# Kernel tuning notes

Measured on AMD Instinct MI355X. Metric: run time of the kernel, lower is better.

Reference implementation:

```python
import jax, jax.numpy as jnp
import numpy as np

N_QUBITS = 12
BATCH = 4096


def _rx(t):
    c = jnp.cos(t / 2).astype(jnp.complex64)
    s = jnp.sin(t / 2).astype(jnp.complex64)
    return jnp.stack([jnp.stack([c, -1j * s], -1), jnp.stack([-1j * s, c], -1)], -2)


def _ry(t):
    c = jnp.cos(t / 2).astype(jnp.complex64)
    s = jnp.sin(t / 2).astype(jnp.complex64)
    return jnp.stack([jnp.stack([c, -s], -1), jnp.stack([s, c], -1)], -2)


def _rz(t):
    e0 = jnp.exp(-0.5j * t.astype(jnp.complex64))
    e1 = jnp.exp(0.5j * t.astype(jnp.complex64))
    z = jnp.zeros_like(e0)
    return jnp.stack([jnp.stack([e0, z], -1), jnp.stack([z, e1], -1)], -2)


ISWAP = jnp.array([[1, 0, 0, 0], [0, 0, 1j, 0], [0, 1j, 0, 0], [0, 0, 0, 1]], dtype=jnp.complex64)


def apply_1q(state, mat, wire):
    # state: [B] + [2]*n, mat: [2,2] or [B,2,2]
    state = jnp.moveaxis(state, wire + 1, 1)
    if mat.ndim == 3:
        state = jnp.einsum('bij,bj...->bi...', mat, state)
    else:
        state = jnp.einsum('ij,bj...->bi...', mat, state)
    return jnp.moveaxis(state, 1, wire + 1)


def apply_2q(state, mat4, w0, w1):
    state = jnp.moveaxis(state, (w0 + 1, w1 + 1), (1, 2))
    shp = state.shape
    state = state.reshape(shp[0], 4, -1)
    state = jnp.einsum('ij,bjr->bir', mat4, state)
    return jnp.moveaxis(state.reshape(shp), (1, 2), (w0 + 1, w1 + 1))


def setup_inputs() -> dict:
    key = jax.random.key(0)
    k1, k2, k3 = jax.random.split(key, 3)
    x = jax.random.normal(k1, (BATCH, 1, 14, 14), dtype=jnp.float32)
    conv_w = jax.random.uniform(k2, (1, 1, 4, 4), jnp.float32, 0.0, 0.1)
    conv_b = jax.random.uniform(k3, (1,), jnp.float32, 0.01, 1.0)
    theta = jnp.full((3,), np.pi / 2, dtype=jnp.float32)  # trainable RX/RY/RZ angles
    return {"x": x, "conv_w": conv_w, "conv_b": conv_b, "theta": theta}


def _circuit(f, theta):
    # f: [B, 36] encoding angles
    B = f.shape[0]
    state = jnp.zeros((B,) + (2,) * N_QUBITS, jnp.complex64)
    state = state.at[(slice(None),) + (0,) * N_QUBITS].set(1.0)
    # encoder1: gates [rx, ry, rx] per qubit, angle = f[:, q*3+i]
    gates1 = (_rx, _ry, _rx)
    for q in range(N_QUBITS):
        for i in range(3):
            state = apply_1q(state, gates1[i](f[:, q * 3 + i]), q)
    # iswap ascending: wires [11,10], [10,9], ..., [1,0]
    for i in range(N_QUBITS - 1):
        state = apply_2q(state, ISWAP, N_QUBITS - i - 1, N_QUBITS - i - 2)
    # encoder2: gates [ry, rx, ry]
    gates2 = (_ry, _rx, _ry)
    for q in range(N_QUBITS):
        for i in range(3):
            state = apply_1q(state, gates2[i](f[:, q * 3 + i]), q)
    # iswap descending: wires [1,0], [2,1], ..., [11,10]
    for i in range(N_QUBITS - 1):
        state = apply_2q(state, ISWAP, i + 1, i)
    # trainable rotations on wires 0 then 1 (shared params)
    for w in (0, 1):
        state = apply_1q(state, _rx(theta[0]), w)
        state = apply_1q(state, _ry(theta[1]), w)
        state = apply_1q(state, _rz(theta[2]), w)
    probs = state.real ** 2 + state.imag ** 2  # [B] + [2]*12
    outs = []
    for w in (0, 1):  # <Z> on wires 0, 1
        p = jnp.moveaxis(probs, w + 1, 1).reshape(B, 2, -1).sum(-1)
        outs.append(p[:, 0] - p[:, 1])
    return jnp.stack(outs, -1)  # [B, 2]


def reference(x, conv_w, conv_b, theta):
    feats = jax.lax.conv_general_dilated(
        x, conv_w, window_strides=(2, 2), padding='VALID',
        dimension_numbers=('NCHW', 'OIHW', 'NCHW')) + conv_b[None, :, None, None]
    f = feats.reshape(x.shape[0], -1)  # [B, 36]
    return _circuit(f, theta)
```

## Files before the change

kernel.cpp:

```cpp
#include <hip/hip_runtime.h>

#define THREADS 64
#define EPB 16

__device__ __forceinline__ float2 cmul(float2 a, float2 b) {
    return make_float2(a.x * b.x - a.y * b.y, a.x * b.y + a.y * b.x);
}
__device__ __forceinline__ float2 cadd(float2 a, float2 b) { return make_float2(a.x + b.x, a.y + b.y); }
__device__ __forceinline__ float2 csub(float2 a, float2 b) { return make_float2(a.x - b.x, a.y - b.y); }
__device__ __forceinline__ float2 conjc(float2 a) { return make_float2(a.x, -a.y); }
__device__ __forceinline__ float2 cmuli(float2 a) { return make_float2(-a.y, a.x); }
__device__ __forceinline__ float2 cdot(float2 a, float2 b) {
    return make_float2(a.x * b.x + a.y * b.y, a.x * b.y - a.y * b.x);
}
__device__ __forceinline__ float2 cscale(float s, float2 a) { return make_float2(s * a.x, s * a.y); }

__device__ __forceinline__ void mat_rx(float c, float s, float2 m[4]) {
    m[0] = make_float2(c, 0.f);  m[1] = make_float2(0.f, -s);
    m[2] = make_float2(0.f, -s); m[3] = make_float2(c, 0.f);
}
__device__ __forceinline__ void mat_ry(float c, float s, float2 m[4]) {
    m[0] = make_float2(c, 0.f);  m[1] = make_float2(-s, 0.f);
    m[2] = make_float2(s, 0.f);  m[3] = make_float2(c, 0.f);
}
__device__ __forceinline__ void mmul(const float2 A[4], const float2 B[4], float2 C[4]) {
    C[0] = cadd(cmul(A[0], B[0]), cmul(A[1], B[2]));
    C[1] = cadd(cmul(A[0], B[1]), cmul(A[1], B[3]));
    C[2] = cadd(cmul(A[2], B[0]), cmul(A[3], B[2]));
    C[3] = cadd(cmul(A[2], B[1]), cmul(A[3], B[3]));
}

__device__ __forceinline__ float2 shfl2(float2 a, int src) {
    return make_float2(__shfl(a.x, src), __shfl(a.y, src));
}
__device__ __forceinline__ float2 shflx2(float2 a, int mask) {
    return make_float2(__shfl_xor(a.x, mask), __shfl_xor(a.y, mask));
}

__global__ __launch_bounds__(THREADS) void qcnn_closed4(
    const float* __restrict__ x,
    const float* __restrict__ cw,
    const float* __restrict__ cb,
    const float* __restrict__ th,
    float* __restrict__ out,
    int B)
{
    __shared__ float xs[EPB][197];

    const int tid = threadIdx.x;
    const int sub = tid & 3;
    const int grp = tid >> 2;
    const int b   = blockIdx.x * EPB + grp;

    const float th0 = th[0], th1 = th[1];

    {
        const float4* xv = (const float4*)(x + (size_t)blockIdx.x * EPB * 196);
        float4 v[12];
#pragma unroll
        for (int k = 0; k < 12; ++k) v[k] = xv[tid + k * THREADS];
        float4 vt;
        if (tid < 16) vt = xv[768 + tid];
#pragma unroll
        for (int k = 0; k < 12; ++k) {
            int i4 = tid + k * THREADS;
            int r  = i4 / 49;
            int c  = (i4 - r * 49) * 4;
            xs[r][c + 0] = v[k].x;
            xs[r][c + 1] = v[k].y;
            xs[r][c + 2] = v[k].z;
            xs[r][c + 3] = v[k].w;
        }
        if (tid < 16) {
            int i4 = 768 + tid;
            int r  = i4 / 49;
            int c  = (i4 - r * 49) * 4;
            xs[r][c + 0] = vt.x;
            xs[r][c + 1] = vt.y;
            xs[r][c + 2] = vt.z;
            xs[r][c + 3] = vt.w;
        }
    }

    float o00; float2 o01;
    {
        float ct0 = __cosf(0.5f * th0), st0v = __sinf(0.5f * th0);
        float ct1 = __cosf(0.5f * th1), st1v = __sinf(0.5f * th1);
        float2 Rx[4], Ry[4], M[4];
        mat_rx(ct0, st0v, Rx); mat_ry(ct1, st1v, Ry); mmul(Ry, Rx, M);
        o00 = (M[0].x * M[0].x + M[0].y * M[0].y)
            - (M[2].x * M[2].x + M[2].y * M[2].y);
        o01 = csub(cmul(conjc(M[0]), M[1]), cmul(conjc(M[2]), M[3]));
    }

    float wgt[16];
#pragma unroll
    for (int k = 0; k < 16; ++k) wgt[k] = cw[k];
    const float bias = cb[0];

    __syncthreads();
    const float* row = xs[grp];

    float ang[9];
#pragma unroll
    for (int m = 0; m < 9; ++m) {
        int o  = sub * 9 + m;
        int oy = o / 6, ox = o % 6;
        float acc = bias;
#pragma unroll
        for (int ky = 0; ky < 4; ++ky)
#pragma unroll
            for (int kx = 0; kx < 4; ++kx)
                acc += row[(2 * oy + ky) * 14 + (2 * ox + kx)] * wgt[ky * 4 + kx];
        ang[m] = acc;
    }

    float2 u[3][2];
    float2 V[3][4];
#pragma unroll
    for (int j = 0; j < 3; ++j) {
        float c0 = __cosf(0.5f * ang[3 * j + 0]), s0 = __sinf(0.5f * ang[3 * j + 0]);
        float c1 = __cosf(0.5f * ang[3 * j + 1]), s1 = __sinf(0.5f * ang[3 * j + 1]);
        float c2 = __cosf(0.5f * ang[3 * j + 2]), s2 = __sinf(0.5f * ang[3 * j + 2]);
        {
            float2 b0c = make_float2(c0, 0.f);
            float2 b1c = make_float2(0.f, -s0);
            float2 t0 = csub(cscale(c1, b0c), cscale(s1, b1c));
            float2 t1 = cadd(cscale(s1, b0c), cscale(c1, b1c));
            u[j][0] = cadd(cscale(c2, t0), cmul(make_float2(0.f, -s2), t1));
            u[j][1] = cadd(cmul(make_float2(0.f, -s2), t0), cscale(c2, t1));
        }
        {
            float2 A[4], Bm[4], Cm[4], T[4];
            mat_ry(c0, s0, A); mat_rx(c1, s1, Bm); mat_ry(c2, s2, Cm);
            mmul(Bm, A, T); mmul(Cm, T, V[j]);
        }
    }

    const int srcPrev = tid - (sub ? 1 : 0);
    float2 up0 = shfl2(u[2][0], srcPrev);
    float2 up1 = shfl2(u[2][1], srcPrev);

    float2 P0p[2][2], P1p[2][2];
#pragma unroll
    for (int v = 0; v < 2; ++v)
#pragma unroll
        for (int vp = 0; vp < 2; ++vp) {
            P0p[v][vp] = make_float2(1.f, 0.f);
            P1p[v][vp] = make_float2(1.f, 0.f);
        }
    float2 V0[4], h9[2][2], h10[2][2];

#pragma unroll
    for (int j = 0; j < 3; ++j) {
        float2 pv0 = (j == 0) ? up0 : u[j - 1][0];
        float2 pv1 = (j == 0) ? up1 : u[j - 1][1];
        float2 hc[2][2];
#pragma unroll
        for (int v = 0; v < 2; ++v) {
            float2 g0 = (v == 0) ? pv0 : cmuli(pv0);
            float2 g1 = (v == 1) ? pv1 : cmuli(pv1);
            hc[v][0] = cadd(cmul(V[j][0], g0), cmul(V[j][1], g1));
            hc[v][1] = cadd(cmul(V[j][2], g0), cmul(V[j][3], g1));
        }
        float2 S[2][2];
#pragma unroll
        for (int v = 0; v < 2; ++v)
#pragma unroll
            for (int vp = 0; vp < 2; ++vp)
                S[v][vp] = cadd(cdot(hc[v][0], hc[vp][0]),
                                cdot(hc[v][1], hc[vp][1]));

        if (sub == 0) {
            if (j == 0) {
#pragma unroll
                for (int k = 0; k < 4; ++k) V0[k] = V[0][k];
            } else if (j == 1) {
#pragma unroll
                for (int v = 0; v < 2; ++v) {
                    h10[v][0] = hc[v][0]; h10[v][1] = hc[v][1];
#pragma unroll
                    for (int vp = 0; vp < 2; ++vp)
                        P1p[v][vp] = cmul(P1p[v][vp], S[v][vp]);
                }
            } else {
#pragma unroll
                for (int v = 0; v < 2; ++v) {
                    h9[v][0] = hc[v][0]; h9[v][1] = hc[v][1];
#pragma unroll
                    for (int vp = 0; vp < 2; ++vp)
                        P0p[v][vp] = cmul(P0p[v][vp], S[v][vp]);
                }
            }
        } else {
#pragma unroll
            for (int v = 0; v < 2; ++v)
#pragma unroll
                for (int vp = 0; vp < 2; ++vp) {
                    P0p[v][vp] = cmul(P0p[v][vp], S[v][vp]);
                    P1p[v][vp] = cmul(P1p[v][vp], S[v][vp]);
                }
        }
    }

#pragma unroll
    for (int d = 1; d <= 2; d <<= 1) {
#pragma unroll
        for (int v = 0; v < 2; ++v)
#pragma unroll
            for (int vp = 0; vp < 2; ++vp) {
                P0p[v][vp] = cmul(P0p[v][vp], shflx2(P0p[v][vp], d));
                P1p[v][vp] = cmul(P1p[v][vp], shflx2(P1p[v][vp], d));
            }
    }

    const int srcLast = tid | 3;
    float2 u11_0 = shfl2(u[2][0], srcLast);
    float2 u11_1 = shfl2(u[2][1], srcLast);

    if (sub == 0) {
        float2 h11[2][2];
        h11[0][0] = cmul(u11_0, V0[0]); h11[0][1] = cmul(u11_0, V0[2]);
        h11[1][0] = cmul(u11_1, V0[1]); h11[1][1] = cmul(u11_1, V0[3]);

        float2 E0 = make_float2(0.f, 0.f), E1 = make_float2(0.f, 0.f);
#pragma unroll
        for (int w = 0; w < 2; ++w) {
            float2 Ow01 = (w == 0) ? cmuli(o01) : make_float2(o01.y, -o01.x);
            float2 Ow10 = conjc(Ow01);
#pragma unroll
            for (int v = 0; v < 2; ++v) {
#pragma unroll
                for (int vp = 0; vp < 2; ++vp) {
                    float2 A = cdot(h11[v][w], h11[vp][w]);
                    float2 T0 = cadd(cadd(
                        cscale(o00, csub(cdot(h10[v][0], h10[vp][0]),
                                         cdot(h10[v][1], h10[vp][1]))),
                        cmul(Ow01, cdot(h10[v][0], h10[vp][1]))),
                        cmul(Ow10, cdot(h10[v][1], h10[vp][0])));
                    float2 T1 = cadd(cadd(
                        cscale(o00, csub(cdot(h9[v][0], h9[vp][0]),
                                         cdot(h9[v][1], h9[vp][1]))),
                        cmul(Ow01, cdot(h9[v][0], h9[vp][1]))),
                        cmul(Ow10, cdot(h9[v][1], h9[vp][0])));
                    E0 = cadd(E0, cmul(cmul(A, T0), P0p[v][vp]));
                    E1 = cadd(E1, cmul(cmul(A, T1), P1p[v][vp]));
                }
            }
        }
        if (b < B)
            ((float2*)out)[b] = make_float2(E0.x, E1.x);
    }
}

extern "C" void kernel_launch(void* const* d_in, const int* in_sizes, int n_in,
                              void* d_out, int out_size, void* d_ws, size_t ws_size,
                              hipStream_t stream) {
    const float* x  = (const float*)d_in[0];
    const float* cw = (const float*)d_in[1];
    const float* cb = (const float*)d_in[2];
    const float* th = (const float*)d_in[3];
    float* out = (float*)d_out;
    int B = in_sizes[0] / 196;
    qcnn_closed4<<<B / EPB, THREADS, 0, stream>>>(x, cw, cb, th, out, B);
}
```

Measured before the change: 11.01 us.

## Load image rows directly into registers instead of staging through shared memory

Each thread now loads the 6 image rows (84 floats) it needs straight from global memory into registers, then computes 12 conv outputs and picks 9 based on sub parity. This removes the shared-memory tile and the __syncthreads barrier. In exchange every row is loaded by several threads, each thread does 12 instead of 9 convolutions, and register pressure rises sharply (84 floats) with uncoalesced per-thread float4 loads.

```diff
diff --git a/kernel.cpp b/kernel.cpp
--- a/kernel.cpp
+++ b/kernel.cpp
@@ -45,43 +45,27 @@
     float* __restrict__ out,
     int B)
 {
-    __shared__ float xs[EPB][197];
-
     const int tid = threadIdx.x;
     const int sub = tid & 3;
     const int grp = tid >> 2;
     const int b   = blockIdx.x * EPB + grp;
 
+    const int r0 = (sub * 3) & ~1;
+    const float* src = x + (size_t)b * 196 + r0 * 14;
+    float arr[84];
+    {
+        const float4* sv = (const float4*)src;
+#pragma unroll
+        for (int k = 0; k < 21; ++k) {
+            float4 v = sv[k];
+            arr[4 * k + 0] = v.x;
+            arr[4 * k + 1] = v.y;
+            arr[4 * k + 2] = v.z;
+            arr[4 * k + 3] = v.w;
+        }
+    }
+
     const float th0 = th[0], th1 = th[1];
-
-    {
-        const float4* xv = (const float4*)(x + (size_t)blockIdx.x * EPB * 196);
-        float4 v[12];
-#pragma unroll
-        for (int k = 0; k < 12; ++k) v[k] = xv[tid + k * THREADS];
-        float4 vt;
-        if (tid < 16) vt = xv[768 + tid];
-#pragma unroll
-        for (int k = 0; k < 12; ++k) {
-            int i4 = tid + k * THREADS;
-            int r  = i4 / 49;
-            int c  = (i4 - r * 49) * 4;
-            xs[r][c + 0] = v[k].x;
-            xs[r][c + 1] = v[k].y;
-            xs[r][c + 2] = v[k].z;
-            xs[r][c + 3] = v[k].w;
-        }
-        if (tid < 16) {
-            int i4 = 768 + tid;
-            int r  = i4 / 49;
-            int c  = (i4 - r * 49) * 4;
-            xs[r][c + 0] = vt.x;
-            xs[r][c + 1] = vt.y;
-            xs[r][c + 2] = vt.z;
-            xs[r][c + 3] = vt.w;
-        }
-    }
-
     float o00; float2 o01;
     {
         float ct0 = __cosf(0.5f * th0), st0v = __sinf(0.5f * th0);
@@ -98,22 +82,23 @@
     for (int k = 0; k < 16; ++k) wgt[k] = cw[k];
     const float bias = cb[0];
 
-    __syncthreads();
-    const float* row = xs[grp];
-
+    float cv[12];
+#pragma unroll
+    for (int mm = 0; mm < 12; ++mm) {
+        const int ry = 2 * (mm / 6), cxx = 2 * (mm % 6);
+        float acc = bias;
+#pragma unroll
+        for (int ky = 0; ky < 4; ++ky)
+#pragma unroll
+            for (int kx = 0; kx < 4; ++kx)
+                acc += arr[(ry + ky) * 14 + cxx + kx] * wgt[ky * 4 + kx];
+        cv[mm] = acc;
+    }
+    const bool oddsub = (sub & 1);
     float ang[9];
 #pragma unroll
-    for (int m = 0; m < 9; ++m) {
-        int o  = sub * 9 + m;
-        int oy = o / 6, ox = o % 6;
-        float acc = bias;
-#pragma unroll
-        for (int ky = 0; ky < 4; ++ky)
-#pragma unroll
-            for (int kx = 0; kx < 4; ++kx)
-                acc += row[(2 * oy + ky) * 14 + (2 * ox + kx)] * wgt[ky * 4 + kx];
-        ang[m] = acc;
-    }
+    for (int m = 0; m < 9; ++m)
+        ang[m] = oddsub ? cv[m + 3] : cv[m];
 
     float2 u[3][2];
     float2 V[3][4];
```

Result: faster. 10.11 us (-8.2%).
